# Optimization experiments

Measured on AMD Instinct MI355X. Metric: run time of the kernel, lower is better.

Reference implementation:

```python
import jax, jax.numpy as jnp
import numpy as np

B, L, D = 4, 2048, 1024
H, DK, DV = 4, 256, 256
CHUNK = 32
MIN_FLOOR, MAX_FLOOR = 0.01, 0.1
EPS = 1e-5


def _l2norm(x):
    return x * jax.lax.rsqrt(jnp.sum(x * x, -1, keepdims=True) + 1e-6)


def _causal_dwconv(x, w):
    # x: [b, L, C], w: [C, k] -> depthwise causal 1d conv
    b, l, c = x.shape
    k = w.shape[-1]
    xt = jnp.transpose(x, (0, 2, 1))
    y = jax.lax.conv_general_dilated(xt, w[:, None, :], (1,), [(k - 1, 0)],
                                     dimension_numbers=('NCH', 'OIH', 'NCH'),
                                     feature_group_count=c)
    return jnp.transpose(y, (0, 2, 1))


def _delta_rule_chunkwise(q, k, v, beta, chunk=CHUNK):
    # q,k: [b,h,L,dk]; v: [b,h,L,dv]; beta: [b,h,L]; L % chunk == 0
    b, h, l, dk = q.shape
    dv = v.shape[-1]
    q = _l2norm(q)
    k = _l2norm(k)
    v = v * beta[..., None]
    kb = k * beta[..., None]
    n = l // chunk
    resh = lambda t: t.reshape(b, h, n, chunk, t.shape[-1])
    q, k, v, kb = resh(q), resh(k), resh(v), resh(kb)
    tri = jnp.triu(jnp.ones((chunk, chunk), bool))        # incl diag
    strict = jnp.triu(jnp.ones((chunk, chunk), bool), 1)  # excl diag
    att = jnp.where(tri, 0.0, -(kb @ jnp.swapaxes(k, -1, -2)))
    # UT transform: forward substitution building (I - lower)^{-1}
    for i in range(1, chunk):
        upd = jnp.einsum('bhnj,bhnjk->bhnk', att[..., i, :], att)
        att = att.at[..., i, :i].add(upd[..., :i])
    att = att + jnp.eye(chunk, dtype=att.dtype)
    u = att @ v
    w = att @ kb

    def step(S, xs):
        q_i, k_i, u_i, w_i = xs  # [b,h,chunk,d]
        local = jnp.where(strict, 0.0, q_i @ jnp.swapaxes(k_i, -1, -2))
        u_adj = u_i - w_i @ S
        o_i = q_i @ S + local @ u_adj
        return S + jnp.swapaxes(k_i, -1, -2) @ u_adj, o_i

    xs = tuple(jnp.moveaxis(t, 2, 0) for t in (q, k, u, w))
    S0 = jnp.zeros((b, h, dk, dv), q.dtype)
    S, o = jax.lax.scan(step, S0, xs)
    return jnp.moveaxis(o, 0, 2).reshape(b, h, l, dv), S


def _rmsnorm(x, w):
    return x * jax.lax.rsqrt(jnp.mean(x * x, -1, keepdims=True) + EPS) * w


def setup_inputs():
    key = jax.random.key(0)
    ks = jax.random.split(key, 16)
    s = 0.02
    return {
        'hidden_states': jax.random.normal(ks[0], (B, L, D), jnp.float32),
        'W_q': jax.random.normal(ks[1], (D, H * DK), jnp.float32) * s,
        'W_k': jax.random.normal(ks[2], (D, H * DK), jnp.float32) * s,
        'W_v': jax.random.normal(ks[3], (D, H * DV), jnp.float32) * s,
        'W_b': jax.random.normal(ks[4], (D, H), jnp.float32) * s,
        'conv_w_q': jax.random.normal(ks[5], (H * DK, 4), jnp.float32) * 0.3,
        'conv_w_k': jax.random.normal(ks[6], (H * DK, 4), jnp.float32) * 0.3,
        'conv_w_v': jax.random.normal(ks[7], (H * DV, 4), jnp.float32) * 0.3,
        'fir_short_w': jax.random.normal(ks[8], (H, DV, 3), jnp.float32) * 0.1,
        'fir_long_w': jax.random.normal(ks[9], (H, DV, 31), jnp.float32) * 0.1,
        'W_fuse1': jax.random.normal(ks[10], (D + 3 * H * DV, 2 * D), jnp.float32) * s,
        'b_fuse1': jnp.zeros((2 * D,), jnp.float32),
        'W_fuse2': jax.random.normal(ks[11], (2 * D, H * 4), jnp.float32) * s,
        'b_fuse2': jnp.zeros((H * 4,), jnp.float32).at[3::4].set(4.0),
        'others_log_tau': jnp.zeros((H,), jnp.float32),
        'norm_w': jnp.ones((DV,), jnp.float32),
        'W_o': jax.random.normal(ks[12], (H * DV, D), jnp.float32) * s,
    }


def reference(hidden_states, W_q, W_k, W_v, W_b, conv_w_q, conv_w_k, conv_w_v,
              fir_short_w, fir_long_w, W_fuse1, b_fuse1, W_fuse2, b_fuse2,
              others_log_tau, norm_w, W_o):
    b, l, d = hidden_states.shape
    # projections + mandatory short conv (silu activation)
    q = jax.nn.silu(_causal_dwconv(hidden_states @ W_q, conv_w_q))
    k = jax.nn.silu(_causal_dwconv(hidden_states @ W_k, conv_w_k))
    v = jax.nn.silu(_causal_dwconv(hidden_states @ W_v, conv_w_v))
    q = q.reshape(b, l, H, DK)
    k = k.reshape(b, l, H, DK)
    v = v.reshape(b, l, H, DV)
    beta = jax.nn.sigmoid(hidden_states @ W_b)  # [b,l,H]
    delta_out, _ = _delta_rule_chunkwise(
        jnp.transpose(q, (0, 2, 1, 3)), jnp.transpose(k, (0, 2, 1, 3)),
        jnp.transpose(v, (0, 2, 1, 3)), jnp.transpose(beta, (0, 2, 1)))
    delta_out = jnp.transpose(delta_out, (0, 2, 1, 3))  # [b,l,H,DV]
    # depthwise FIR paths on v
    vc = v.reshape(b, l, H * DV)
    fir_s = _causal_dwconv(vc, fir_short_w.reshape(H * DV, -1)).reshape(b, l, H, DV)
    fir_l = _causal_dwconv(vc, fir_long_w.reshape(H * DV, -1)).reshape(b, l, H, DV)
    # fusion gate MLP
    gate_in = jnp.concatenate([hidden_states, fir_s.reshape(b, l, -1),
                               fir_l.reshape(b, l, -1), delta_out.reshape(b, l, -1)], -1)
    hid = jax.nn.gelu(gate_in @ W_fuse1 + b_fuse1, approximate=False)
    logits = (hid @ W_fuse2 + b_fuse2).reshape(b, l, H, 4)
    p_raw = jax.nn.sigmoid(logits[..., 3])
    # token-adaptive context floor
    floor = MIN_FLOOR + (MAX_FLOOR - MIN_FLOOR) * (1.0 - p_raw)
    p_val = (1.0 - floor) * p_raw
    tau = jnp.exp(others_log_tau)  # per-head temperature
    others = jax.nn.softmax(logits[..., :3] / tau[None, None, :, None], -1)
    p_ctx = (1.0 - p_val)[..., None] * others
    o = (p_ctx[..., 0:1] * fir_s + p_ctx[..., 1:2] * fir_l +
         p_ctx[..., 2:3] * delta_out + p_val[..., None] * v)
    o = _rmsnorm(o, norm_w)
    return o.reshape(b, l, H * DV) @ W_o
```

## Files before the change

### kernel.cpp

```cpp
#include <hip/hip_runtime.h>
#include <hip/hip_bf16.h>

#define B_ 4
#define L_ 2048
#define D_ 1024
#define H_ 4
#define DK_ 256
#define DV_ 256
#define NCH 64
#define NTOK 8192

typedef __attribute__((ext_vector_type(8))) short bf16x8;
typedef __attribute__((ext_vector_type(4))) float f32x4;
typedef unsigned int u32;

__device__ __forceinline__ float bu2f(unsigned short u) {
    union { unsigned int i; float f; } x; x.i = ((unsigned int)u) << 16; return x.f;
}
__device__ __forceinline__ unsigned short f2bu(float f) {
    union { __hip_bfloat16 h; unsigned short u; } x; x.h = __float2bfloat16(f); return x.u;
}
#define MFMA16(a, b, c) __builtin_amdgcn_mfma_f32_16x16x32_bf16(a, b, c, 0, 0, 0)

__device__ __forceinline__ void gload16(const void* g, void* l) {
    __builtin_amdgcn_global_load_lds(
        (const __attribute__((address_space(1))) u32*)g,
        (__attribute__((address_space(3))) u32*)l, 16, 0, 0);
}

__global__ __launch_bounds__(256) void k_transpose(const float* __restrict__ in,
                                                   unsigned short* __restrict__ out,
                                                   int K, int N) {
    __shared__ float tile[32][33];
    int k0 = blockIdx.y * 32, n0 = blockIdx.x * 32;
    int tx = threadIdx.x & 31, ty = threadIdx.x >> 5;
#pragma unroll
    for (int r = 0; r < 4; ++r)
        tile[ty + 8 * r][tx] = in[(long)(k0 + ty + 8 * r) * N + n0 + tx];
    __syncthreads();
#pragma unroll
    for (int r = 0; r < 4; ++r)
        out[(long)(n0 + ty + 8 * r) * K + k0 + tx] = f2bu(tile[tx][ty + 8 * r]);
}

__global__ __launch_bounds__(256) void k_padT2(const float* __restrict__ W,
                                               unsigned short* __restrict__ out) {
    long idx = (long)blockIdx.x * 256 + threadIdx.x;
    int n = (int)(idx >> 11), k = (int)(idx & 2047);
    out[idx] = (n < 16) ? f2bu(W[k * 16 + n]) : (unsigned short)0;
}

__global__ __launch_bounds__(256) void k_cvt_hs(const float4* __restrict__ hs4,
                                                unsigned short* __restrict__ gate_in) {
    int idx = blockIdx.x * 256 + threadIdx.x;
    float4 v = hs4[idx];
    int row = idx >> 8;
    int c4 = (idx & 255) * 4;
    ushort4 o;
    o.x = f2bu(v.x); o.y = f2bu(v.y); o.z = f2bu(v.z); o.w = f2bu(v.w);
    *reinterpret_cast<ushort4*>(&gate_in[(long)row * 4096 + c4]) = o;
}

__global__ __launch_bounds__(64) void k_beta(const float* __restrict__ hs,
                                             const float* __restrict__ W_b,
                                             float* __restrict__ beta) {
    int tok = blockIdx.x;
    int lane = threadIdx.x;
    const float* hrow = hs + (long)tok * D_;
    float acc0 = 0, acc1 = 0, acc2 = 0, acc3 = 0;
    for (int c = lane; c < D_; c += 64) {
        float x = hrow[c];
        float4 wb = reinterpret_cast<const float4*>(W_b)[c];
        acc0 += x * wb.x; acc1 += x * wb.y; acc2 += x * wb.z; acc3 += x * wb.w;
    }
#pragma unroll
    for (int off = 32; off; off >>= 1) {
        acc0 += __shfl_down(acc0, off);
        acc1 += __shfl_down(acc1, off);
        acc2 += __shfl_down(acc2, off);
        acc3 += __shfl_down(acc3, off);
    }
    if (lane == 0) {
        int b = tok >> 11, l = tok & 2047;
        beta[((long)(b * H_ + 0)) * L_ + l] = 1.f / (1.f + expf(-acc0));
        beta[((long)(b * H_ + 1)) * L_ + l] = 1.f / (1.f + expf(-acc1));
        beta[((long)(b * H_ + 2)) * L_ + l] = 1.f / (1.f + expf(-acc2));
        beta[((long)(b * H_ + 3)) * L_ + l] = 1.f / (1.f + expf(-acc3));
    }
}

template <int EPI>
__global__ __launch_bounds__(256) void k_gemm(const unsigned short* __restrict__ A, int lda,
                                              const unsigned short* __restrict__ BT, int ldb,
                                              void* __restrict__ Cout, int ldc,
                                              const float* __restrict__ bias,
                                              int K, int gx) {
    __shared__ __align__(16) unsigned short As[128][64];
    __shared__ __align__(16) unsigned short Bs[128][64];
    const int tid = threadIdx.x;
    const int wave = tid >> 6, lane = tid & 63;
    const int wm = wave & 1, wn = wave >> 1;
    const int lr = lane & 15, lg = lane >> 4;
    const int nwg = gridDim.x;
    const int cpx = nwg >> 3;
    const int orig = blockIdx.x;
    const int wg = (orig & 7) * cpx + (orig >> 3);
    const int m0 = (wg / gx) * 128, n0 = (wg % gx) * 128;
    const int srow = wave * 32 + (lane >> 3);
    const int scol = (((lane & 7) ^ ((lane >> 3) & 7))) * 8;
    const unsigned short* Ap = &A[(long)(m0 + srow) * lda + scol];
    const unsigned short* Bp = &BT[(long)(n0 + srow) * ldb + scol];
    unsigned short* AsB = &As[wave * 32][0];
    unsigned short* BsB = &Bs[wave * 32][0];
    const unsigned short* AsF = &As[0][0];
    const unsigned short* BsF = &Bs[0][0];
    f32x4 acc[4][4] = {};
    for (int k0 = 0; k0 < K; k0 += 64) {
#pragma unroll
        for (int g = 0; g < 4; ++g) {
            gload16(Ap + (long)g * 8 * lda + k0, AsB + g * 8 * 64);
            gload16(Bp + (long)g * 8 * ldb + k0, BsB + g * 8 * 64);
        }
        __syncthreads();
#pragma unroll
        for (int ks = 0; ks < 2; ++ks) {
            bf16x8 af[4], bfr[4];
#pragma unroll
            for (int mt = 0; mt < 4; ++mt) {
                int r = wm * 64 + mt * 16 + lr;
                af[mt] = *reinterpret_cast<const bf16x8*>(
                    AsF + r * 64 + (((ks * 4 + lg) ^ (lr & 7)) * 8));
            }
#pragma unroll
            for (int nt = 0; nt < 4; ++nt) {
                int r = wn * 64 + nt * 16 + lr;
                bfr[nt] = *reinterpret_cast<const bf16x8*>(
                    BsF + r * 64 + (((ks * 4 + lg) ^ (lr & 7)) * 8));
            }
#pragma unroll
            for (int mt = 0; mt < 4; ++mt)
#pragma unroll
                for (int nt = 0; nt < 4; ++nt)
                    acc[mt][nt] = MFMA16(af[mt], bfr[nt], acc[mt][nt]);
        }
        __syncthreads();
    }
#pragma unroll
    for (int mt = 0; mt < 4; ++mt)
#pragma unroll
        for (int nt = 0; nt < 4; ++nt)
#pragma unroll
            for (int r = 0; r < 4; ++r) {
                int row = m0 + wm * 64 + mt * 16 + lg * 4 + r;
                int col = n0 + wn * 64 + nt * 16 + lr;
                float v = acc[mt][nt][r];
                if (EPI == 2) {
                    v += bias[col];
                    v = 0.5f * v * (1.f + erff(v * 0.70710678118f));
                }
                if (EPI == 0)
                    reinterpret_cast<float*>(Cout)[(long)row * ldc + col] = v;
                else
                    reinterpret_cast<unsigned short*>(Cout)[(long)row * ldc + col] = f2bu(v);
            }
}

__global__ __launch_bounds__(256) void k_conv_silu(const unsigned short* __restrict__ QKVp,
                                                   const float* __restrict__ cwq,
                                                   const float* __restrict__ cwk,
                                                   const float* __restrict__ cwv,
                                                   unsigned short* __restrict__ qn,
                                                   unsigned short* __restrict__ kn,
                                                   unsigned short* __restrict__ v_blc) {
    int tok = blockIdx.x;
    int b = tok >> 11, l = tok & 2047;
    int t = threadIdx.x;
    float y[12];
#pragma unroll
    for (int j = 0; j < 12; ++j) {
        int c = t + 256 * j;
        const float* cw = (j < 4) ? &cwq[c * 4] : (j < 8) ? &cwk[(c - 1024) * 4] : &cwv[(c - 2048) * 4];
        float s = 0.f;
#pragma unroll
        for (int jj = 0; jj < 4; ++jj) {
            int tl = l - 3 + jj;
            if (tl >= 0) s += bu2f(QKVp[((long)(b * L_ + tl)) * 3072 + c]) * cw[jj];
        }
        y[j] = s / (1.f + expf(-s));
    }
    float sq[8];
#pragma unroll
    for (int j = 0; j < 8; ++j) sq[j] = y[j] * y[j];
    int wave = t >> 6, lane = t & 63;
#pragma unroll
    for (int off = 32; off; off >>= 1)
#pragma unroll
        for (int j = 0; j < 8; ++j) sq[j] += __shfl_down(sq[j], off);
    __shared__ float red[4][8];
    if (lane == 0)
#pragma unroll
        for (int j = 0; j < 8; ++j) red[wave][j] = sq[j];
    __syncthreads();
    float tot[8];
#pragma unroll
    for (int j = 0; j < 8; ++j) tot[j] = red[0][j] + red[1][j] + red[2][j] + red[3][j];
#pragma unroll
    for (int h = 0; h < 4; ++h) {
        float sc = rsqrtf(tot[h] + 1e-6f);
        qn[((long)(b * H_ + h) * L_ + l) * 256 + t] = f2bu(y[h] * sc);
    }
#pragma unroll
    for (int h = 0; h < 4; ++h) {
        float sc = rsqrtf(tot[4 + h] + 1e-6f);
        kn[((long)(b * H_ + h) * L_ + l) * 256 + t] = f2bu(y[4 + h] * sc);
    }
#pragma unroll
    for (int h = 0; h < 4; ++h)
        v_blc[(long)tok * 1024 + h * 256 + t] = f2bu(y[8 + h]);
}

__global__ __launch_bounds__(256) void k_delta_chunk(const unsigned short* __restrict__ qn,
                                                     const unsigned short* __restrict__ kn,
                                                     const unsigned short* __restrict__ v_blc,
                                                     const float* __restrict__ beta,
                                                     unsigned short* __restrict__ u_buf,
                                                     unsigned short* __restrict__ w_buf,
                                                     unsigned short* __restrict__ local_buf,
                                                     unsigned short* __restrict__ kT_buf) {
    int bid = blockIdx.x;
    int n = bid & 63, bh = bid >> 6;
    int b = bh >> 2, h = bh & 3;
    int t0 = n * 32;
    __shared__ __align__(16) unsigned short k_s[32][264];
    __shared__ __align__(16) unsigned short vbT[256][40];
    __shared__ __align__(16) unsigned short kbT[256][40];
    __shared__ __align__(16) float att[32][33];
    __shared__ __align__(16) unsigned short att_b[32][40];
    __shared__ float bet[32];
    int tid = threadIdx.x, wave = tid >> 6, lane = tid & 63;
    int lr = lane & 15, lg = lane >> 4;

    {
        int row = tid >> 3;
        int cc = (tid & 7) * 32;
        float brow = beta[(long)bh * L_ + t0 + row];
        if ((tid & 7) == 0) bet[row] = brow;
        const uint4* kp = reinterpret_cast<const uint4*>(&kn[((long)bh * L_ + t0 + row) * 256 + cc]);
        const uint4* vp = reinterpret_cast<const uint4*>(&v_blc[((long)(b * L_ + t0 + row)) * 1024 + h * 256 + cc]);
        unsigned short kv[32], vv[32];
#pragma unroll
        for (int g = 0; g < 4; ++g) {
            uint4 x = kp[g];
            *reinterpret_cast<uint4*>(&kv[g * 8]) = x;
            *reinterpret_cast<uint4*>(&k_s[row][cc + g * 8]) = x;
            *reinterpret_cast<uint4*>(&vv[g * 8]) = vp[g];
        }
#pragma unroll
        for (int e = 0; e < 32; ++e) {
            kbT[cc + e][row] = f2bu(bu2f(kv[e]) * brow);
            vbT[cc + e][row] = f2bu(bu2f(vv[e]) * brow);
        }
    }
    __syncthreads();

    {
        unsigned short tmp[32];
#pragma unroll
        for (int t = 0; t < 32; ++t) tmp[t] = k_s[t][tid];
#pragma unroll
        for (int g = 0; g < 4; ++g)
            *reinterpret_cast<uint4*>(&kT_buf[((long)bid * 256 + tid) * 32 + g * 8]) =
                *reinterpret_cast<uint4*>(&tmp[g * 8]);
    }

    {
        int i0 = (wave & 1) * 16, j0 = (wave >> 1) * 16;
        f32x4 G = {0, 0, 0, 0}, S2 = {0, 0, 0, 0};
#pragma unroll
        for (int kk = 0; kk < 8; ++kk) {
            bf16x8 bk = *reinterpret_cast<const bf16x8*>(&k_s[j0 + lr][kk * 32 + lg * 8]);
            bf16x8 ak = *reinterpret_cast<const bf16x8*>(&k_s[i0 + lr][kk * 32 + lg * 8]);
            bf16x8 aq = *reinterpret_cast<const bf16x8*>(&qn[((long)bh * L_ + t0 + i0 + lr) * 256 + kk * 32 + lg * 8]);
            G = MFMA16(ak, bk, G);
            S2 = MFMA16(aq, bk, S2);
        }
#pragma unroll
        for (int r = 0; r < 4; ++r) {
            int i = i0 + lg * 4 + r, j = j0 + lr;
            att[i][j] = (j < i) ? -bet[i] * G[r] : 0.f;
            local_buf[(long)bid * 1024 + i * 32 + j] = f2bu((j <= i) ? S2[r] : 0.f);
        }
    }
    __syncthreads();

    for (int i = 1; i < 32; ++i) {
        float upd = 0.f;
        if (tid < i) {
            for (int j = tid + 1; j < i; ++j) upd += att[i][j] * att[j][tid];
        }
        __syncthreads();
        if (tid < i) att[i][tid] += upd;
        __syncthreads();
    }
    for (int e = tid; e < 1024; e += 256) {
        int i = e >> 5, j = e & 31;
        att_b[i][j] = f2bu(att[i][j] + ((i == j) ? 1.f : 0.f));
    }
    __syncthreads();

    {
        int mt = wave & 1;
        bf16x8 afr = *reinterpret_cast<const bf16x8*>(&att_b[mt * 16 + lr][lg * 8]);
        f32x4 z = {0, 0, 0, 0};
#pragma unroll
        for (int ntt = 0; ntt < 8; ++ntt) {
            int n0c = (wave >> 1) * 128 + ntt * 16;
            bf16x8 bu = *reinterpret_cast<const bf16x8*>(&vbT[n0c + lr][lg * 8]);
            bf16x8 bw = *reinterpret_cast<const bf16x8*>(&kbT[n0c + lr][lg * 8]);
            f32x4 ut = MFMA16(afr, bu, z);
            f32x4 wt = MFMA16(afr, bw, z);
#pragma unroll
            for (int r = 0; r < 4; ++r) {
                int t = mt * 16 + lg * 4 + r, c = n0c + lr;
                u_buf[((long)bid * 32 + t) * 256 + c] = f2bu(ut[r]);
                w_buf[((long)bid * 32 + t) * 256 + c] = f2bu(wt[r]);
            }
        }
    }
}

__global__ __launch_bounds__(256) void k_scan(const unsigned short* __restrict__ qn,
                                              const unsigned short* __restrict__ u_buf,
                                              const unsigned short* __restrict__ w_buf,
                                              const unsigned short* __restrict__ local_buf,
                                              const unsigned short* __restrict__ kT_buf,
                                              unsigned short* __restrict__ gate_in) {
    int bid = blockIdx.x;
    int bh = bid & 15, dvb = bid >> 4;
    int b = bh >> 2, h = bh & 3;
    int dc0 = dvb * 16;
    __shared__ __align__(16) unsigned short Tb[16][264];
    __shared__ __align__(16) unsigned short uaT[16][40];
    const int tid = threadIdx.x, wave = tid >> 6, lane = tid & 63;
    const int lr = lane & 15, lg = lane >> 4;
    const int wi = wave & 1;
    const bool isW = wave < 2;
    const int c0w = wave * 64;
    f32x4 Tacc[4] = {};
    for (int e = tid; e < 16 * 264; e += 256) (&Tb[0][0])[e] = 0;
    const unsigned short* q_bh = qn + (long)bh * L_ * 256;
    const unsigned short* u_bh = u_buf + (long)bh * 64 * 8192;
    const unsigned short* w_bh = w_buf + (long)bh * 64 * 8192;
    const unsigned short* l_bh = local_buf + (long)bh * 64 * 1024;
    const unsigned short* kT_bh = kT_buf + (long)bh * 64 * 8192;
    const unsigned short* wq_base = (isW ? w_bh : q_bh) + (16 * wi + lr) * 256;
    const unsigned short* u_base = u_bh + (16 * wi + lg * 4) * 256 + dc0 + lr;
    const unsigned short* l_base = l_bh + (16 * wi + lr) * 32 + lg * 8;
    const unsigned short* kT_base = kT_bh + (c0w + lr) * 32 + lg * 8;
    bf16x8 wqA[8], kB[4], lA = {};
    float uv[4];
    auto prefetch = [&](int n) {
        long o8 = (long)n * 8192;
#pragma unroll
        for (int kk = 0; kk < 8; ++kk)
            wqA[kk] = *reinterpret_cast<const bf16x8*>(wq_base + o8 + kk * 32 + lg * 8);
#pragma unroll
        for (int cc = 0; cc < 4; ++cc)
            kB[cc] = *reinterpret_cast<const bf16x8*>(kT_base + o8 + cc * 512);
        if (isW) {
#pragma unroll
            for (int r = 0; r < 4; ++r) uv[r] = bu2f(u_base[o8 + r * 256]);
        } else {
            lA = *reinterpret_cast<const bf16x8*>(l_base + (long)n * 1024);
        }
    };
    prefetch(0);
    __syncthreads();
    for (int n = 0; n < 64; ++n) {
        f32x4 P0 = {0, 0, 0, 0}, P1 = {0, 0, 0, 0};
#pragma unroll
        for (int kk = 0; kk < 8; kk += 2) {
            bf16x8 t0 = *reinterpret_cast<const bf16x8*>(&Tb[lr][kk * 32 + lg * 8]);
            bf16x8 t1 = *reinterpret_cast<const bf16x8*>(&Tb[lr][(kk + 1) * 32 + lg * 8]);
            P0 = MFMA16(wqA[kk], t0, P0);
            P1 = MFMA16(wqA[kk + 1], t1, P1);
        }
        f32x4 P;
#pragma unroll
        for (int r = 0; r < 4; ++r) P[r] = P0[r] + P1[r];
        if (isW) {
#pragma unroll
            for (int r = 0; r < 4; ++r)
                uaT[lr][16 * wi + lg * 4 + r] = f2bu(uv[r] - P[r]);
        }
        bf16x8 kBc[4];
#pragma unroll
        for (int cc = 0; cc < 4; ++cc) kBc[cc] = kB[cc];
        bf16x8 lAc = lA;
        if (n + 1 < 64) prefetch(n + 1);
        __syncthreads();
        bf16x8 uaA = *reinterpret_cast<const bf16x8*>(&uaT[lr][lg * 8]);
        if (!isW) {
            f32x4 O = MFMA16(lAc, uaA, P);
#pragma unroll
            for (int r = 0; r < 4; ++r) {
                long row = (long)b * L_ + n * 32 + 16 * wi + lg * 4 + r;
                gate_in[row * 4096 + 3072 + h * 256 + dc0 + lr] = f2bu(O[r]);
            }
        }
#pragma unroll
        for (int cc = 0; cc < 4; ++cc)
            Tacc[cc] = MFMA16(uaA, kBc[cc], Tacc[cc]);
#pragma unroll
        for (int cc = 0; cc < 4; ++cc)
#pragma unroll
            for (int r = 0; r < 4; ++r)
                Tb[lg * 4 + r][c0w + cc * 16 + lr] = f2bu(Tacc[cc][r]);
        __syncthreads();
    }
}

__global__ __launch_bounds__(256) void k_fir(const unsigned short* __restrict__ v_blc,
                                             const float* __restrict__ ws3,
                                             const float* __restrict__ wl31,
                                             unsigned short* __restrict__ gate_in) {
    __shared__ unsigned short xs[94][256];
    int b = blockIdx.y, tt = blockIdx.x * 64, c0 = blockIdx.z * 256;
    int tid = threadIdx.x;
    for (int r = 0; r < 94; ++r) {
        int t = tt - 30 + r;
        xs[r][tid] = (t >= 0) ? v_blc[((long)(b * L_ + t)) * 1024 + c0 + tid] : (unsigned short)0;
    }
    int c = c0 + tid;
    float wl[31], ws[3];
#pragma unroll
    for (int j = 0; j < 31; ++j) wl[j] = wl31[(long)c * 31 + j];
#pragma unroll
    for (int j = 0; j < 3; ++j) ws[j] = ws3[(long)c * 3 + j];
    __syncthreads();
    for (int t = 0; t < 64; ++t) {
        float accl = 0.f, accs = 0.f;
#pragma unroll
        for (int j = 0; j < 31; ++j) accl += bu2f(xs[t + j][tid]) * wl[j];
#pragma unroll
        for (int j = 0; j < 3; ++j) accs += bu2f(xs[t + 28 + j][tid]) * ws[j];
        long row = (long)b * L_ + tt + t;
        gate_in[row * 4096 + 1024 + c] = f2bu(accs);
        gate_in[row * 4096 + 2048 + c] = f2bu(accl);
    }
}

__global__ __launch_bounds__(256) void k_gate(const float* __restrict__ logits_pre,
                                              const float* __restrict__ b_fuse2,
                                              const float* __restrict__ log_tau,
                                              const float* __restrict__ norm_w,
                                              const unsigned short* __restrict__ gate_in,
                                              const unsigned short* __restrict__ v_blc,
                                              unsigned short* __restrict__ o_norm) {
    int tok = blockIdx.x;
    int tid = threadIdx.x;
    __shared__ float lg_s[16];
    __shared__ float red[4][4];
    if (tid < 16) lg_s[tid] = logits_pre[(long)tok * 128 + tid] + b_fuse2[tid];
    __syncthreads();
    float o[4];
#pragma unroll
    for (int h = 0; h < 4; ++h) {
        float l0 = lg_s[h * 4 + 0], l1 = lg_s[h * 4 + 1], l2 = lg_s[h * 4 + 2], l3 = lg_s[h * 4 + 3];
        float praw = 1.f / (1.f + expf(-l3));
        float fl_ = 0.01f + 0.09f * (1.f - praw);
        float pval = (1.f - fl_) * praw;
        float itau = expf(-log_tau[h]);
        float a0 = l0 * itau, a1 = l1 * itau, a2 = l2 * itau;
        float m = fmaxf(a0, fmaxf(a1, a2));
        float e0 = expf(a0 - m), e1 = expf(a1 - m), e2 = expf(a2 - m);
        float inv = (1.f - pval) / (e0 + e1 + e2);
        long base = (long)tok * 4096;
        float fs = bu2f(gate_in[base + 1024 + h * 256 + tid]);
        float flv = bu2f(gate_in[base + 2048 + h * 256 + tid]);
        float dd = bu2f(gate_in[base + 3072 + h * 256 + tid]);
        float vv = bu2f(v_blc[(long)tok * 1024 + h * 256 + tid]);
        o[h] = e0 * inv * fs + e1 * inv * flv + e2 * inv * dd + pval * vv;
    }
    int wave = tid >> 6, lane = tid & 63;
    float s[4];
#pragma unroll
    for (int h = 0; h < 4; ++h) s[h] = o[h] * o[h];
#pragma unroll
    for (int off = 32; off; off >>= 1)
#pragma unroll
        for (int h = 0; h < 4; ++h) s[h] += __shfl_down(s[h], off);
    if (lane == 0)
#pragma unroll
        for (int h = 0; h < 4; ++h) red[wave][h] = s[h];
    __syncthreads();
#pragma unroll
    for (int h = 0; h < 4; ++h) {
        float tot = red[0][h] + red[1][h] + red[2][h] + red[3][h];
        float sc = rsqrtf(tot * (1.f / 256.f) + 1e-5f);
        o_norm[(long)tok * 1024 + h * 256 + tid] = f2bu(o[h] * sc * norm_w[tid]);
    }
}

extern "C" void kernel_launch(void* const* d_in, const int* in_sizes, int n_in,
                              void* d_out, int out_size, void* d_ws, size_t ws_size,
                              hipStream_t stream) {
    const float* hs = (const float*)d_in[0];
    const float* W_q = (const float*)d_in[1];
    const float* W_k = (const float*)d_in[2];
    const float* W_v = (const float*)d_in[3];
    const float* W_b = (const float*)d_in[4];
    const float* cwq = (const float*)d_in[5];
    const float* cwk = (const float*)d_in[6];
    const float* cwv = (const float*)d_in[7];
    const float* fir_s_w = (const float*)d_in[8];
    const float* fir_l_w = (const float*)d_in[9];
    const float* W_f1 = (const float*)d_in[10];
    const float* b_f1 = (const float*)d_in[11];
    const float* W_f2 = (const float*)d_in[12];
    const float* b_f2 = (const float*)d_in[13];
    const float* log_tau = (const float*)d_in[14];
    const float* norm_w = (const float*)d_in[15];
    const float* W_o = (const float*)d_in[16];

    char* ws = (char*)d_ws;
    size_t off = 0;
    auto alloc = [&](size_t bytes) { size_t o = off; off += (bytes + 255) & ~(size_t)255; return o; };
    unsigned short* gate_in = (unsigned short*)(ws + alloc((size_t)NTOK * 4096 * 2));
    unsigned short* QKVp    = (unsigned short*)(ws + alloc((size_t)NTOK * 3072 * 2));
    unsigned short* WqkvT   = (unsigned short*)(ws + alloc((size_t)3072 * 1024 * 2));
    unsigned short* Wf1T    = (unsigned short*)(ws + alloc((size_t)2048 * 4096 * 2));
    unsigned short* WoT     = (unsigned short*)(ws + alloc((size_t)1024 * 1024 * 2));
    unsigned short* Wf2Tp   = (unsigned short*)(ws + alloc((size_t)128 * 2048 * 2));
    float*          beta    = (float*)(ws + alloc((size_t)16 * 2048 * 4));
    unsigned short* qn      = (unsigned short*)(ws + alloc((size_t)16 * 2048 * 256 * 2));
    unsigned short* kn      = (unsigned short*)(ws + alloc((size_t)16 * 2048 * 256 * 2));
    unsigned short* v_blc   = (unsigned short*)(ws + alloc((size_t)NTOK * 1024 * 2));
    unsigned short* u_buf   = (unsigned short*)(ws + alloc((size_t)16 * 64 * 8192 * 2));
    unsigned short* w_buf   = (unsigned short*)(ws + alloc((size_t)16 * 64 * 8192 * 2));
    unsigned short* locb    = (unsigned short*)(ws + alloc((size_t)16 * 64 * 1024 * 2));
    unsigned short* kT_buf  = (unsigned short*)(ws + alloc((size_t)16 * 64 * 8192 * 2));
    float*          logits  = (float*)(ws + alloc((size_t)NTOK * 128 * 4));
    unsigned short* o_norm  = (unsigned short*)(ws + alloc((size_t)NTOK * 1024 * 2));
    unsigned short* hid     = QKVp;

    k_transpose<<<dim3(32, 32), 256, 0, stream>>>(W_q, WqkvT, 1024, 1024);
    k_transpose<<<dim3(32, 32), 256, 0, stream>>>(W_k, WqkvT + (size_t)1024 * 1024, 1024, 1024);
    k_transpose<<<dim3(32, 32), 256, 0, stream>>>(W_v, WqkvT + (size_t)2048 * 1024, 1024, 1024);
    k_transpose<<<dim3(64, 128), 256, 0, stream>>>(W_f1, Wf1T, 4096, 2048);
    k_transpose<<<dim3(32, 32), 256, 0, stream>>>(W_o, WoT, 1024, 1024);
    k_padT2<<<1024, 256, 0, stream>>>(W_f2, Wf2Tp);
    k_cvt_hs<<<8192, 256, 0, stream>>>((const float4*)hs, gate_in);
    k_beta<<<8192, 64, 0, stream>>>(hs, W_b, beta);
    k_gemm<1><<<24 * 64, 256, 0, stream>>>(gate_in, 4096, WqkvT, 1024, QKVp, 3072, nullptr,
                                           1024, 24);
    k_conv_silu<<<8192, 256, 0, stream>>>(QKVp, cwq, cwk, cwv, qn, kn, v_blc);
    k_delta_chunk<<<1024, 256, 0, stream>>>(qn, kn, v_blc, beta, u_buf, w_buf, locb, kT_buf);
    k_scan<<<256, 256, 0, stream>>>(qn, u_buf, w_buf, locb, kT_buf, gate_in);
    k_fir<<<dim3(32, 4, 4), 256, 0, stream>>>(v_blc, fir_s_w, fir_l_w, gate_in);
    k_gemm<2><<<16 * 64, 256, 0, stream>>>(gate_in, 4096, Wf1T, 4096, hid, 2048, b_f1,
                                           4096, 16);
    k_gemm<0><<<1 * 64, 256, 0, stream>>>(hid, 2048, Wf2Tp, 2048, logits, 128, nullptr,
                                          2048, 1);
    k_gate<<<8192, 256, 0, stream>>>(logits, b_f2, log_tau, norm_w, gate_in, v_blc, o_norm);
    k_gemm<0><<<8 * 64, 256, 0, stream>>>(o_norm, 1024, WoT, 1024, (float*)d_out, 1024, nullptr,
                                          1024, 8);
}
```

Baseline: 732.1 us.

## Add 256x256 double-buffered GEMM kernel for QKV and fusion-MLP projections

Introduces a new 512-thread GEMM with 256x256 output tiles, double-buffered LDS staging, XOR-swizzled shared layout, and an interleaved load/MFMA schedule with priority hints. It replaces the 128x128 GEMM for the QKV projection and the first fusion-gate MLP layer. Larger tiles raise arithmetic intensity and reuse, and the prefetch overlaps global loads with compute. The trade-offs are fewer workgroups per launch (384 and 256), a large register footprint (32 accumulator vectors per thread), and 128KB of LDS per block, which may limit occupancy.

```diff
diff --git a/kernel.cpp b/kernel.cpp
--- a/kernel.cpp
+++ b/kernel.cpp
@@ -87,6 +87,125 @@
         beta[((long)(b * H_ + 2)) * L_ + l] = 1.f / (1.f + expf(-acc2));
         beta[((long)(b * H_ + 3)) * L_ + l] = 1.f / (1.f + expf(-acc3));
     }
+}
+
+template <int EPI>
+__global__ __launch_bounds__(512, 2) void k_gemm256(const unsigned short* __restrict__ A, int lda,
+                                                    const unsigned short* __restrict__ BT, int ldb,
+                                                    void* __restrict__ Cout, int ldc,
+                                                    const float* __restrict__ bias,
+                                                    int K, int gx) {
+    __shared__ __align__(16) unsigned short As[2][256][64];
+    __shared__ __align__(16) unsigned short Bs[2][256][64];
+    const int tid = threadIdx.x;
+    const int wave = tid >> 6, lane = tid & 63;
+    const int lr = lane & 15, lg = lane >> 4;
+    const int sl = lane >> 3;
+    const int sg = ((lane & 7) ^ (sl & 7)) * 8;
+    const int nwg = gridDim.x, cpx = nwg >> 3, orig = blockIdx.x;
+    const int wg = (orig & 7) * cpx + (orig >> 3);
+    const int m0 = (wg / gx) * 256, n0 = (wg % gx) * 256;
+    const unsigned short* Abase = A + (long)(m0 + wave * 8 + sl) * lda + sg;
+    const unsigned short* Bbase = BT + (long)(n0 + wave * 8 + sl) * ldb + sg;
+    f32x4 acc[16][2] = {};
+    const int NT = K >> 6;
+
+#define STG_A(h, nb, k0s) { \
+    gload16(Abase + (long)((h) * 128) * lda + (k0s), &As[nb][(h) * 128 + wave * 8][0]); \
+    gload16(Abase + (long)((h) * 128 + 64) * lda + (k0s), &As[nb][(h) * 128 + 64 + wave * 8][0]); }
+#define STG_B(h, nb, k0s) { \
+    gload16(Bbase + (long)((h) * 128) * ldb + (k0s), &Bs[nb][(h) * 128 + wave * 8][0]); \
+    gload16(Bbase + (long)((h) * 128 + 64) * ldb + (k0s), &Bs[nb][(h) * 128 + 64 + wave * 8][0]); }
+#define LDA_F(dst, mt, ks) dst = *reinterpret_cast<const bf16x8*>( \
+    &As[sb][(mt) * 16 + lr][(((ks) * 4 + lg) ^ (lr & 7)) * 8]);
+#define LDB_F(dst, nt, ks) dst = *reinterpret_cast<const bf16x8*>( \
+    &Bs[sb][wave * 32 + (nt) * 16 + lr][(((ks) * 4 + lg) ^ (lr & 7)) * 8]);
+#define BARRIER() { asm volatile("" ::: "memory"); __builtin_amdgcn_s_barrier(); \
+                    asm volatile("" ::: "memory"); }
+#define DO_MFMA(p) { \
+    __builtin_amdgcn_s_setprio(1); \
+    _Pragma("unroll") for (int i = 0; i < 4; ++i) \
+        _Pragma("unroll") for (int nt = 0; nt < 2; ++nt) { \
+            acc[(p) * 4 + i][nt] = MFMA16(a[i][0], bfr[nt][0], acc[(p) * 4 + i][nt]); \
+            acc[(p) * 4 + i][nt] = MFMA16(a[i][1], bfr[nt][1], acc[(p) * 4 + i][nt]); } \
+    __builtin_amdgcn_s_setprio(0); }
+
+    STG_B(0, 0, 0) STG_B(1, 0, 0) STG_A(0, 0, 0) STG_A(1, 0, 0)
+    asm volatile("s_waitcnt vmcnt(2)" ::: "memory");
+    BARRIER()
+
+    bf16x8 bfr[2][2];
+    for (int t = 0; t < NT; ++t) {
+        const int sb = t & 1, nb = sb ^ 1;
+        const int k0s = (t + 1) << 6;
+        const bool more = (t + 1) < NT;
+        {
+            if (more) STG_B(0, nb, k0s)
+            bf16x8 a[4][2];
+            LDB_F(bfr[0][0], 0, 0) LDB_F(bfr[0][1], 0, 1)
+            LDB_F(bfr[1][0], 1, 0) LDB_F(bfr[1][1], 1, 1)
+#pragma unroll
+            for (int i = 0; i < 4; ++i) { LDA_F(a[i][0], 0 * 4 + i, 0) LDA_F(a[i][1], 0 * 4 + i, 1) }
+            BARRIER()
+            DO_MFMA(0)
+            BARRIER()
+        }
+        {
+            if (more) STG_B(1, nb, k0s)
+            bf16x8 a[4][2];
+#pragma unroll
+            for (int i = 0; i < 4; ++i) { LDA_F(a[i][0], 1 * 4 + i, 0) LDA_F(a[i][1], 1 * 4 + i, 1) }
+            if (more) { asm volatile("s_waitcnt vmcnt(4)" ::: "memory"); }
+            else      { asm volatile("s_waitcnt vmcnt(0)" ::: "memory"); }
+            BARRIER()
+            DO_MFMA(1)
+            BARRIER()
+        }
+        {
+            if (more) STG_A(0, nb, k0s)
+            bf16x8 a[4][2];
+#pragma unroll
+            for (int i = 0; i < 4; ++i) { LDA_F(a[i][0], 2 * 4 + i, 0) LDA_F(a[i][1], 2 * 4 + i, 1) }
+            BARRIER()
+            DO_MFMA(2)
+            BARRIER()
+        }
+        {
+            if (more) STG_A(1, nb, k0s)
+            bf16x8 a[4][2];
+#pragma unroll
+            for (int i = 0; i < 4; ++i) { LDA_F(a[i][0], 3 * 4 + i, 0) LDA_F(a[i][1], 3 * 4 + i, 1) }
+            if (more) { asm volatile("s_waitcnt vmcnt(2)" ::: "memory"); }
+            else      { asm volatile("s_waitcnt vmcnt(0)" ::: "memory"); }
+            BARRIER()
+            DO_MFMA(3)
+            BARRIER()
+        }
+    }
+#undef STG_A
+#undef STG_B
+#undef LDA_F
+#undef LDB_F
+#undef BARRIER
+#undef DO_MFMA
+#pragma unroll
+    for (int mt = 0; mt < 16; ++mt)
+#pragma unroll
+        for (int nt = 0; nt < 2; ++nt)
+#pragma unroll
+            for (int r = 0; r < 4; ++r) {
+                int row = m0 + mt * 16 + lg * 4 + r;
+                int col = n0 + wave * 32 + nt * 16 + lr;
+                float v = acc[mt][nt][r];
+                if (EPI == 2) {
+                    v += bias[col];
+                    v = 0.5f * v * (1.f + erff(v * 0.70710678118f));
+                }
+                if (EPI == 0)
+                    reinterpret_cast<float*>(Cout)[(long)row * ldc + col] = v;
+                else
+                    reinterpret_cast<unsigned short*>(Cout)[(long)row * ldc + col] = f2bu(v);
+            }
 }
 
 template <int EPI>
@@ -552,14 +671,14 @@
     k_padT2<<<1024, 256, 0, stream>>>(W_f2, Wf2Tp);
     k_cvt_hs<<<8192, 256, 0, stream>>>((const float4*)hs, gate_in);
     k_beta<<<8192, 64, 0, stream>>>(hs, W_b, beta);
-    k_gemm<1><<<24 * 64, 256, 0, stream>>>(gate_in, 4096, WqkvT, 1024, QKVp, 3072, nullptr,
-                                           1024, 24);
+    k_gemm256<1><<<32 * 12, 512, 0, stream>>>(gate_in, 4096, WqkvT, 1024, QKVp, 3072, nullptr,
+                                              1024, 12);
     k_conv_silu<<<8192, 256, 0, stream>>>(QKVp, cwq, cwk, cwv, qn, kn, v_blc);
     k_delta_chunk<<<1024, 256, 0, stream>>>(qn, kn, v_blc, beta, u_buf, w_buf, locb, kT_buf);
     k_scan<<<256, 256, 0, stream>>>(qn, u_buf, w_buf, locb, kT_buf, gate_in);
     k_fir<<<dim3(32, 4, 4), 256, 0, stream>>>(v_blc, fir_s_w, fir_l_w, gate_in);
-    k_gemm<2><<<16 * 64, 256, 0, stream>>>(gate_in, 4096, Wf1T, 4096, hid, 2048, b_f1,
-                                           4096, 16);
+    k_gemm256<2><<<32 * 8, 512, 0, stream>>>(gate_in, 4096, Wf1T, 4096, hid, 2048, b_f1,
+                                             4096, 8);
     k_gemm<0><<<1 * 64, 256, 0, stream>>>(hid, 2048, Wf2Tp, 2048, logits, 128, nullptr,
                                           2048, 1);
     k_gate<<<8192, 256, 0, stream>>>(logits, b_f2, log_tau, norm_w, gate_in, v_blc, o_norm);
```

Measured after the change: 794.5 us. +8.5%, slower.
